# Performance work log

Measured on AMD Instinct MI355X. Metric: run time of the kernel, lower is better.

The kernel has to match this reference:

```python
import jax, jax.numpy as jnp
import numpy as np

B, C, CI, H, W = 4, 256, 128, 64, 64
BN_EPS = 1e-5

def _proj(t, w, b):
    # 1x1 conv == channel-mixing GEMM
    return jnp.einsum('bchw,oc->bohw', t, w) + b[None, :, None, None]

def setup_inputs() -> dict:
    key = jax.random.key(0)
    ks = jax.random.split(key, 16)
    d = {
        'x': jax.random.normal(ks[0], (B, C, H, W), jnp.float32),
        'y': jax.random.normal(ks[1], (B, C, H, W), jnp.float32),
        'z': jax.random.normal(ks[2], (B, C, H, W), jnp.float32),
        'theta_w': jax.random.normal(ks[3], (CI, C), jnp.float32) * 0.02,
        'theta_b': jax.random.normal(ks[4], (CI,), jnp.float32) * 0.02,
        'phi_w': jax.random.normal(ks[5], (CI, C), jnp.float32) * 0.02,
        'phi_b': jax.random.normal(ks[6], (CI,), jnp.float32) * 0.02,
        'g_w': jax.random.normal(ks[7], (CI, C), jnp.float32) * 0.02,
        'g_b': jax.random.normal(ks[8], (CI,), jnp.float32) * 0.02,
        'w_w': jax.random.normal(ks[9], (C, CI), jnp.float32) * 0.02,
        'w_b': jax.random.normal(ks[10], (C,), jnp.float32) * 0.02,
        'bn_gamma': jax.random.normal(ks[11], (C,), jnp.float32) * 0.1 + 1.0,
        'bn_beta': jax.random.normal(ks[12], (C,), jnp.float32) * 0.1,
        'bn_mean': jax.random.normal(ks[13], (C,), jnp.float32) * 0.1,
        'bn_var': jax.random.uniform(ks[14], (C,), jnp.float32, 0.5, 1.5),
    }
    return d

def reference(x, y, z, theta_w, theta_b, phi_w, phi_b, g_w, g_b,
              w_w, w_b, bn_gamma, bn_beta, bn_mean, bn_var):
    b, c, h, w = x.shape
    n = h * w
    theta_x = _proj(x, theta_w, theta_b).reshape(b, CI, n).transpose(0, 2, 1)  # [B,N,Ci]
    phi_y = _proj(y, phi_w, phi_b).reshape(b, CI, n)                           # [B,Ci,N]
    f = jnp.einsum('bnc,bcm->bnm', theta_x, phi_y)                             # [B,N,N]
    f_div_c = jax.nn.softmax(f, axis=-1)
    g_z = _proj(z, g_w, g_b).reshape(b, CI, n).transpose(0, 2, 1)              # [B,N,Ci]
    o = jnp.einsum('bnm,bmc->bnc', f_div_c, g_z)                               # [B,N,Ci]
    o = o.transpose(0, 2, 1).reshape(b, CI, h, w)
    w_y = _proj(o, w_w, w_b)
    # BatchNorm2d (eval mode with running stats)
    inv = bn_gamma / jnp.sqrt(bn_var + BN_EPS)
    w_y = (w_y - bn_mean[None, :, None, None]) * inv[None, :, None, None] + bn_beta[None, :, None, None]
    return w_y + z
```

## Files before the change

### kernel.cpp

```cpp
#include <hip/hip_runtime.h>

typedef unsigned short u16;
typedef unsigned int u32;
typedef short s8v __attribute__((ext_vector_type(8)));
typedef float f16v __attribute__((ext_vector_type(16)));

#define NHW 4096
#define CIN 256
#define CID 128
#define PB  524288

__device__ __forceinline__ u16 f2bf(float f) {
  union { float f; u32 u; } v; v.f = f;
  u32 r = v.u + 0x7fffu + ((v.u >> 16) & 1u);
  return (u16)(r >> 16);
}
__device__ __forceinline__ u32 pk2(float a, float b) {
  return (u32)f2bf(a) | ((u32)f2bf(b) << 16);
}
__device__ __forceinline__ int SIG(int reg, int h) {
  return (reg & 3) + 8 * (reg >> 2) + 4 * h;
}


__global__ __launch_bounds__(256) void wprep_kernel(
    const float* __restrict__ tw, const float* __restrict__ pw, const float* __restrict__ gw,
    const float* __restrict__ ww, const float* __restrict__ wb,
    const float* __restrict__ bg, const float* __restrict__ bb,
    const float* __restrict__ bm, const float* __restrict__ bv,
    u16* __restrict__ Wf, u16* __restrict__ Wf2,
    float* __restrict__ scl, float* __restrict__ offs)
{
  const int bid = blockIdx.x, t = threadIdx.x;
  const int lm = t & 31, h = (t >> 5) & 1, g4 = t >> 6;
  if (bid < 12) {
    const int p = bid >> 2, ct = bid & 3;
    const float* W = (p == 0) ? tw : (p == 1) ? pw : gw;
#pragma unroll
    for (int q = 0; q < 4; ++q) {
      const int ksg = g4 * 4 + q;
      const float* src = W + (size_t)(ct * 32 + lm) * 256 + ksg * 16 + h * 8;
      u32 pk[4];
#pragma unroll
      for (int e = 0; e < 4; ++e) pk[e] = pk2(src[2 * e], src[2 * e + 1]);
      *(uint4*)(Wf + p * 32768 + ct * 8192 + ksg * 512 + h * 256 + lm * 8) =
          make_uint4(pk[0], pk[1], pk[2], pk[3]);
    }
  } else if (bid < 20) {
    const int ct = bid - 12;
#pragma unroll
    for (int q = 0; q < 2; ++q) {
      const int ks = g4 * 2 + q;
      const float* src = ww + (size_t)(ct * 32 + lm) * 128 + ks * 16 + h * 8;
      u32 pk[4];
#pragma unroll
      for (int e = 0; e < 4; ++e) pk[e] = pk2(src[2 * e], src[2 * e + 1]);
      *(uint4*)(Wf2 + ct * 8192 + ks * 512 + h * 256 + lm * 8) =
          make_uint4(pk[0], pk[1], pk[2], pk[3]);
    }
  } else {
    float inv = bg[t] * __frsqrt_rn(bv[t] + 1e-5f);
    scl[t] = inv;
    offs[t] = (wb[t] - bm[t]) * inv + bb[t];
  }
}

__global__ __launch_bounds__(256) void proj_kernel(
    const float* __restrict__ x, const float* __restrict__ y, const float* __restrict__ zz,
    const u16* __restrict__ Wf,
    const float* __restrict__ tb, const float* __restrict__ pb, const float* __restrict__ gb,
    u16* __restrict__ Qf, u16* __restrict__ Kf, u16* __restrict__ Vf)
{
  __shared__ __align__(16) u16 Xs[64 * 64];
  __shared__ float Bs[128];
  const int t = threadIdx.x;
  const int b = blockIdx.y, p = blockIdx.z;
  const int n0 = blockIdx.x * 64;
  const float* in  = (p == 0) ? x  : (p == 1) ? y  : zz;
  const float* Bv  = (p == 0) ? tb : (p == 1) ? pb : gb;
  u16*         out = (p == 0) ? Qf : (p == 1) ? Kf : Vf;
  const u16* Wfp = Wf + p * 32768;

  const int wave = t >> 6, lane = t & 63;
  const int lm = lane & 31, h = lane >> 5;
  const int nt = wave & 1, ctp = wave >> 1;
  const int cp = t >> 3, noct = t & 7;

  if (t < 128) Bs[t] = Bv[t];

  u32* Xd = (u32*)Xs;
  const int nn = nt * 32 + lm;
  const int rmask = ((nn >> 3) & 7) << 2;

  f16v a0, a1;
#pragma unroll
  for (int r = 0; r < 16; ++r) { a0[r] = 0.f; a1[r] = 0.f; }

  float4 xr[4];
  {
    const float* basep = in + ((size_t)(b * CIN) + 2 * cp) * NHW + n0;
    xr[0] = *(const float4*)(basep + noct * 4);
    xr[1] = *(const float4*)(basep + 32 + noct * 4);
    xr[2] = *(const float4*)(basep + NHW + noct * 4);
    xr[3] = *(const float4*)(basep + NHW + 32 + noct * 4);
  }

  for (int ch = 0; ch < 4; ++ch) {
    __syncthreads();
    {
      const float* xa = (const float*)&xr[0];
      const float* xb = (const float*)&xr[1];
      const float* xc = (const float*)&xr[2];
      const float* xd = (const float*)&xr[3];
#pragma unroll
      for (int i = 0; i < 4; ++i) {
        int n1 = noct * 4 + i, n2 = n1 + 32;
        Xd[n1 * 32 + (cp ^ (((n1 >> 3) & 7) << 2))] = pk2(xa[i], xc[i]);
        Xd[n2 * 32 + (cp ^ (((n2 >> 3) & 7) << 2))] = pk2(xb[i], xd[i]);
      }
    }
    __syncthreads();
    if (ch < 3) {
      const float* basep = in + ((size_t)(b * CIN) + (ch + 1) * 64 + 2 * cp) * NHW + n0;
      xr[0] = *(const float4*)(basep + noct * 4);
      xr[1] = *(const float4*)(basep + 32 + noct * 4);
      xr[2] = *(const float4*)(basep + NHW + noct * 4);
      xr[3] = *(const float4*)(basep + NHW + 32 + noct * 4);
    }
    if (p < 2) {
#pragma unroll
      for (int ks = 0; ks < 4; ++ks) {
        s8v xf = *(const s8v*)(Xd + nn * 32 + ((ks * 8 + h * 4) ^ rmask));
        s8v w0 = *(const s8v*)(Wfp + (ctp * 2 + 0) * 8192 + (ch * 4 + ks) * 512 + h * 256 + lm * 8);
        s8v w1 = *(const s8v*)(Wfp + (ctp * 2 + 1) * 8192 + (ch * 4 + ks) * 512 + h * 256 + lm * 8);
        a0 = __builtin_amdgcn_mfma_f32_32x32x16_bf16(w0, xf, a0, 0, 0, 0);
        a1 = __builtin_amdgcn_mfma_f32_32x32x16_bf16(w1, xf, a1, 0, 0, 0);
      }
    } else {
#pragma unroll
      for (int ks = 0; ks < 4; ++ks) {
        s8v xf = *(const s8v*)(Xd + nn * 32 + ((ks * 8 + h * 4) ^ rmask));
        s8v w0 = *(const s8v*)(Wfp + (ctp * 2 + 0) * 8192 + (ch * 4 + ks) * 512 + h * 256 + lm * 8);
        s8v w1 = *(const s8v*)(Wfp + (ctp * 2 + 1) * 8192 + (ch * 4 + ks) * 512 + h * 256 + lm * 8);
        a0 = __builtin_amdgcn_mfma_f32_32x32x16_bf16(xf, w0, a0, 0, 0, 0);
        a1 = __builtin_amdgcn_mfma_f32_32x32x16_bf16(xf, w1, a1, 0, 0, 0);
      }
    }
  }

  const size_t nblk = (size_t)blockIdx.x * 2 + nt;
  if (p < 2) {
#pragma unroll
    for (int cti = 0; cti < 2; ++cti) {
      const int ct = ctp * 2 + cti;
      const f16v& ac = cti ? a1 : a0;
      float v[16];
#pragma unroll
      for (int reg = 0; reg < 16; ++reg) v[reg] = ac[reg] + Bs[ct * 32 + SIG(reg, h)];
      u32 pk[8];
#pragma unroll
      for (int e = 0; e < 8; ++e) pk[e] = pk2(v[2 * e], v[2 * e + 1]);
      u16* dst = out + (size_t)b * PB + nblk * 4096 + ct * 1024 + h * 512 + lm * 16;
      ((uint4*)dst)[0] = make_uint4(pk[0], pk[1], pk[2], pk[3]);
      ((uint4*)dst)[1] = make_uint4(pk[4], pk[5], pk[6], pk[7]);
    }
  } else {
#pragma unroll
    for (int cti = 0; cti < 2; ++cti) {
      const int ct = ctp * 2 + cti;
      const f16v& ac = cti ? a1 : a0;
      const float bias = Bs[ct * 32 + lm];
      u32 pk[8];
#pragma unroll
      for (int e = 0; e < 8; ++e) pk[e] = pk2(ac[2 * e] + bias, ac[2 * e + 1] + bias);
      u16* dst = out + (size_t)b * PB + nblk * 4096 + ct * 1024 + h * 256 + lm * 8;
      *(uint4*)dst         = make_uint4(pk[0], pk[1], pk[2], pk[3]);
      *(uint4*)(dst + 512) = make_uint4(pk[4], pk[5], pk[6], pk[7]);
    }
  }
}

__global__ __launch_bounds__(256, 2) void attn_kernel(
    const u16* __restrict__ Qf, const u16* __restrict__ Kf,
    const u16* __restrict__ Vf, u16* __restrict__ Of)
{
  __shared__ __align__(16) float Obuf[32][132];
  __shared__ float lbuf[32];
  const int t = threadIdx.x;
  const int wave = t >> 6, lane = t & 63;
  const int lm = lane & 31, half = lane >> 5;
  const int b = blockIdx.y;

  s8v qf[8];
  {
    const u16* qp = Qf + (size_t)b * PB + (size_t)blockIdx.x * 4096 + lm * 16 + half * 8;
#pragma unroll
    for (int ks = 0; ks < 8; ++ks) qf[ks] = *(const s8v*)(qp + ks * 512);
  }

  const u16* Kb = Kf + (size_t)b * PB + lm * 16 + half * 8;
  const u16* Vb = Vf + (size_t)b * PB + half * 256 + lm * 8;
  const int mstart = wave * 1024;

  f16v oacc[4];
#pragma unroll
  for (int c = 0; c < 4; ++c)
#pragma unroll
    for (int r = 0; r < 16; ++r) oacc[c][r] = 0.f;
  float lacc = 0.f;

  s8v kf[8];
  {
    const u16* kp = Kb + (size_t)mstart * 128;
#pragma unroll
    for (int ks = 0; ks < 8; ++ks) kf[ks] = *(const s8v*)(kp + ks * 512);
  }

  for (int jt = 0; jt < 32; ++jt) {
    const int m0 = mstart + jt * 32;

    s8v vf[8];
    {
      const u16* vp = Vb + (size_t)m0 * 128;
#pragma unroll
      for (int ct = 0; ct < 4; ++ct)
#pragma unroll
        for (int ks = 0; ks < 2; ++ks)
          vf[ct * 2 + ks] = *(const s8v*)(vp + ct * 1024 + ks * 512);
    }

    f16v sacc;
#pragma unroll
    for (int r = 0; r < 16; ++r) sacc[r] = 0.f;
#pragma unroll
    for (int ks = 0; ks < 8; ++ks)
      sacc = __builtin_amdgcn_mfma_f32_32x32x16_bf16(kf[ks], qf[ks], sacc, 0, 0, 0);

    {
      const u16* kp = Kb + (size_t)(m0 + 32) * 128;
#pragma unroll
      for (int ks = 0; ks < 8; ++ks) kf[ks] = *(const s8v*)(kp + ks * 512);
    }

    union { s8v v; u16 e[8]; } pa0, pa1;
#pragma unroll
    for (int j = 0; j < 8; ++j) {
      float p0 = __expf(sacc[j]);
      float p1 = __expf(sacc[8 + j]);
      lacc += p0 + p1;
      pa0.e[j] = f2bf(p0);
      pa1.e[j] = f2bf(p1);
    }

#pragma unroll
    for (int ct = 0; ct < 4; ++ct) {
      oacc[ct] = __builtin_amdgcn_mfma_f32_32x32x16_bf16(pa0.v, vf[ct * 2 + 0], oacc[ct], 0, 0, 0);
      oacc[ct] = __builtin_amdgcn_mfma_f32_32x32x16_bf16(pa1.v, vf[ct * 2 + 1], oacc[ct], 0, 0, 0);
    }
  }

  lacc += __shfl_xor(lacc, 32);

  __syncthreads();
  if (wave == 0) {
#pragma unroll
    for (int ct = 0; ct < 4; ++ct)
#pragma unroll
      for (int reg = 0; reg < 16; ++reg)
        Obuf[SIG(reg, half)][ct * 32 + lm] = oacc[ct][reg];
    if (half == 0) lbuf[lm] = lacc;
  }
  __syncthreads();
  if (wave != 0) {
#pragma unroll
    for (int ct = 0; ct < 4; ++ct)
#pragma unroll
      for (int reg = 0; reg < 16; ++reg)
        atomicAdd(&Obuf[SIG(reg, half)][ct * 32 + lm], oacc[ct][reg]);
    if (half == 0) atomicAdd(&lbuf[lm], lacc);
  }
  __syncthreads();

  {
    const float inv = 1.0f / lbuf[lm];
    u16* ob = Of + (size_t)b * PB + (size_t)blockIdx.x * 4096 + half * 256 + lm * 8;
#pragma unroll
    for (int kss = 0; kss < 2; ++kss) {
      const int ks = wave * 2 + kss;
      float4 va = *(const float4*)&Obuf[lm][ks * 16 + half * 8];
      float4 vb = *(const float4*)&Obuf[lm][ks * 16 + half * 8 + 4];
      uint4 pk = make_uint4(pk2(va.x * inv, va.y * inv), pk2(va.z * inv, va.w * inv),
                            pk2(vb.x * inv, vb.y * inv), pk2(vb.z * inv, vb.w * inv));
      *(uint4*)(ob + ks * 512) = pk;
    }
  }
}

__global__ __launch_bounds__(256) void outproj_kernel(
    const u16* __restrict__ Of, const float* __restrict__ zz,
    const u16* __restrict__ Wf2, const float* __restrict__ scl,
    const float* __restrict__ offs, float* __restrict__ out)
{
  __shared__ float SC[256], OFS[256];
  const int t = threadIdx.x;
  const int wave = t >> 6, lane = t & 63;
  const int lm = lane & 31, h = lane >> 5;
  const int b = blockIdx.y;
  const int n0 = blockIdx.x * 32;

  SC[t] = scl[t];
  OFS[t] = offs[t];
  __syncthreads();

  s8v of[8];
  {
    const u16* op = Of + (size_t)b * PB + (size_t)blockIdx.x * 4096 + h * 256 + lm * 8;
#pragma unroll
    for (int ks = 0; ks < 8; ++ks) of[ks] = *(const s8v*)(op + ks * 512);
  }

  f16v a0, a1;
#pragma unroll
  for (int r = 0; r < 16; ++r) { a0[r] = 0.f; a1[r] = 0.f; }

  const u16* w2a = Wf2 + (wave * 2 + 0) * 8192 + h * 256 + lm * 8;
  const u16* w2b = Wf2 + (wave * 2 + 1) * 8192 + h * 256 + lm * 8;
#pragma unroll
  for (int ks = 0; ks < 8; ++ks) {
    s8v wa = *(const s8v*)(w2a + ks * 512);
    s8v wb = *(const s8v*)(w2b + ks * 512);
    a0 = __builtin_amdgcn_mfma_f32_32x32x16_bf16(wa, of[ks], a0, 0, 0, 0);
    a1 = __builtin_amdgcn_mfma_f32_32x32x16_bf16(wb, of[ks], a1, 0, 0, 0);
  }

#pragma unroll
  for (int cti = 0; cti < 2; ++cti) {
    const int ct = wave * 2 + cti;
    const f16v& ac = cti ? a1 : a0;
#pragma unroll
    for (int reg = 0; reg < 16; ++reg) {
      const int co = ct * 32 + SIG(reg, h);
      const size_t idx = ((size_t)(b * CIN + co)) * NHW + n0 + lm;
      out[idx] = ac[reg] * SC[co] + OFS[co] + zz[idx];
    }
  }
}

extern "C" void kernel_launch(void* const* d_in, const int* in_sizes, int n_in,
                              void* d_out, int out_size, void* d_ws, size_t ws_size,
                              hipStream_t stream) {
  const float* x  = (const float*)d_in[0];
  const float* y  = (const float*)d_in[1];
  const float* z  = (const float*)d_in[2];
  const float* tw = (const float*)d_in[3];
  const float* tb = (const float*)d_in[4];
  const float* pw = (const float*)d_in[5];
  const float* pb = (const float*)d_in[6];
  const float* gw = (const float*)d_in[7];
  const float* gb = (const float*)d_in[8];
  const float* ww = (const float*)d_in[9];
  const float* wb = (const float*)d_in[10];
  const float* bn_g = (const float*)d_in[11];
  const float* bn_b = (const float*)d_in[12];
  const float* bn_m = (const float*)d_in[13];
  const float* bn_v = (const float*)d_in[14];

  const size_t B = 4;
  const size_t qkv = B * PB;
  char* ws = (char*)d_ws;
  u16* Qf = (u16*)ws;
  u16* Kf = Qf + qkv;
  u16* Vf = Kf + qkv;
  u16* Of = Vf + qkv;
  u16* Wf = Of + qkv;
  u16* Wf2 = Wf + 3 * 32768;
  float* scl  = (float*)(Wf2 + 65536);
  float* offs = scl + 256;

  float* out = (float*)d_out;

  wprep_kernel<<<21, 256, 0, stream>>>(tw, pw, gw, ww, wb, bn_g, bn_b, bn_m, bn_v,
                                       Wf, Wf2, scl, offs);
  proj_kernel<<<dim3(NHW / 64, B, 3), 256, 0, stream>>>(
      x, y, z, Wf, tb, pb, gb, Qf, Kf, Vf);
  attn_kernel<<<dim3(NHW / 32, B), 256, 0, stream>>>(Qf, Kf, Vf, Of);
  outproj_kernel<<<dim3(NHW / 32, B), 256, 0, stream>>>(
      Of, z, Wf2, scl, offs, out);
}
```

Measured before the change: 202.0 us.

## Pre-convert inputs to bf16 fragments and split attention over 8 waves

Adds an xprep kernel that converts x, y, z to bf16 in MFMA fragment layout through an LDS transpose. The projection kernel then loads operands straight from global memory, with no LDS staging or barriers. Separately, the attention kernel moves from 256 to 512 threads, so each wave covers half as many key tiles and the epilogue stores are spread across 8 waves. The cost is an extra kernel launch, an extra round trip of the converted inputs through memory, and more atomic reductions in LDS; the output buffer and the X workspace are reused as scratch.

```diff
diff --git a/kernel.cpp b/kernel.cpp
--- a/kernel.cpp
+++ b/kernel.cpp
@@ -9,6 +9,7 @@
 #define CIN 256
 #define CID 128
 #define PB  524288
+#define XSZ 1048576
 
 __device__ __forceinline__ u16 f2bf(float f) {
   union { float f; u32 u; } v; v.f = f;
@@ -65,86 +66,84 @@
   }
 }
 
+__global__ __launch_bounds__(256) void xprep_kernel(
+    const float* __restrict__ x, const float* __restrict__ y, const float* __restrict__ zz,
+    u16* __restrict__ X0, u16* __restrict__ X1, u16* __restrict__ X2)
+{
+  __shared__ __align__(16) float Xs[128][68];
+  const int t = threadIdx.x;
+  const int b = blockIdx.y, p = blockIdx.z;
+  const int n0 = blockIdx.x * 64;
+  const float* in = (p == 0) ? x : (p == 1) ? y : zz;
+  u16* Xf = ((p == 0) ? X0 : (p == 1) ? X1 : X2) + (size_t)b * XSZ +
+            (size_t)blockIdx.x * 2 * 8192;
+  const int lm = t & 31, h = (t >> 5) & 1, nb = (t >> 6) & 1, q = t >> 7;
+  const int cr = t >> 4, ns = t & 15;
+
+  for (int pass = 0; pass < 2; ++pass) {
+    if (pass) __syncthreads();
+#pragma unroll
+    for (int is = 0; is < 8; ++is) {
+      int c = pass * 128 + is * 16 + cr;
+      *(float4*)&Xs[is * 16 + cr][ns * 4] =
+          *(const float4*)(in + (size_t)(b * CIN + c) * NHW + n0 + ns * 4);
+    }
+    __syncthreads();
+#pragma unroll
+    for (int i = 0; i < 4; ++i) {
+      const int ksgl = q * 4 + i;
+      const int c0 = ksgl * 16 + h * 8;
+      float v[8];
+#pragma unroll
+      for (int j = 0; j < 8; ++j) v[j] = Xs[c0 + j][nb * 32 + lm];
+      uint4 pk = make_uint4(pk2(v[0], v[1]), pk2(v[2], v[3]),
+                            pk2(v[4], v[5]), pk2(v[6], v[7]));
+      *(uint4*)(Xf + nb * 8192 + (pass * 8 + ksgl) * 512 + h * 256 + lm * 8) = pk;
+    }
+  }
+}
+
 __global__ __launch_bounds__(256) void proj_kernel(
-    const float* __restrict__ x, const float* __restrict__ y, const float* __restrict__ zz,
+    const u16* __restrict__ X0, const u16* __restrict__ X1, const u16* __restrict__ X2,
     const u16* __restrict__ Wf,
     const float* __restrict__ tb, const float* __restrict__ pb, const float* __restrict__ gb,
     u16* __restrict__ Qf, u16* __restrict__ Kf, u16* __restrict__ Vf)
 {
-  __shared__ __align__(16) u16 Xs[64 * 64];
   __shared__ float Bs[128];
   const int t = threadIdx.x;
   const int b = blockIdx.y, p = blockIdx.z;
-  const int n0 = blockIdx.x * 64;
-  const float* in  = (p == 0) ? x  : (p == 1) ? y  : zz;
-  const float* Bv  = (p == 0) ? tb : (p == 1) ? pb : gb;
-  u16*         out = (p == 0) ? Qf : (p == 1) ? Kf : Vf;
-  const u16* Wfp = Wf + p * 32768;
-
-  const int wave = t >> 6, lane = t & 63;
-  const int lm = lane & 31, h = lane >> 5;
-  const int nt = wave & 1, ctp = wave >> 1;
-  const int cp = t >> 3, noct = t & 7;
-
+  const float* Bv = (p == 0) ? tb : (p == 1) ? pb : gb;
+  u16* out = (p == 0) ? Qf : (p == 1) ? Kf : Vf;
+  const int wave = t >> 6, lane = t & 63, lm = lane & 31, h = lane >> 5;
+  const int nt = wave & 1, cih = wave >> 1;
   if (t < 128) Bs[t] = Bv[t];
-
-  u32* Xd = (u32*)Xs;
-  const int nn = nt * 32 + lm;
-  const int rmask = ((nn >> 3) & 7) << 2;
+  __syncthreads();
+
+  const u16* Xb = ((p == 0) ? X0 : (p == 1) ? X1 : X2) + (size_t)b * XSZ +
+                  ((size_t)blockIdx.x * 2 + nt) * 8192 + lane * 8;
+  const u16* Wb = Wf + p * 32768 + cih * 2 * 8192 + lane * 8;
 
   f16v a0, a1;
 #pragma unroll
   for (int r = 0; r < 16; ++r) { a0[r] = 0.f; a1[r] = 0.f; }
 
-  float4 xr[4];
-  {
-    const float* basep = in + ((size_t)(b * CIN) + 2 * cp) * NHW + n0;
-    xr[0] = *(const float4*)(basep + noct * 4);
-    xr[1] = *(const float4*)(basep + 32 + noct * 4);
-    xr[2] = *(const float4*)(basep + NHW + noct * 4);
-    xr[3] = *(const float4*)(basep + NHW + 32 + noct * 4);
-  }
-
-  for (int ch = 0; ch < 4; ++ch) {
-    __syncthreads();
-    {
-      const float* xa = (const float*)&xr[0];
-      const float* xb = (const float*)&xr[1];
-      const float* xc = (const float*)&xr[2];
-      const float* xd = (const float*)&xr[3];
-#pragma unroll
-      for (int i = 0; i < 4; ++i) {
-        int n1 = noct * 4 + i, n2 = n1 + 32;
-        Xd[n1 * 32 + (cp ^ (((n1 >> 3) & 7) << 2))] = pk2(xa[i], xc[i]);
-        Xd[n2 * 32 + (cp ^ (((n2 >> 3) & 7) << 2))] = pk2(xb[i], xd[i]);
-      }
-    }
-    __syncthreads();
-    if (ch < 3) {
-      const float* basep = in + ((size_t)(b * CIN) + (ch + 1) * 64 + 2 * cp) * NHW + n0;
-      xr[0] = *(const float4*)(basep + noct * 4);
-      xr[1] = *(const float4*)(basep + 32 + noct * 4);
-      xr[2] = *(const float4*)(basep + NHW + noct * 4);
-      xr[3] = *(const float4*)(basep + NHW + 32 + noct * 4);
-    }
-    if (p < 2) {
-#pragma unroll
-      for (int ks = 0; ks < 4; ++ks) {
-        s8v xf = *(const s8v*)(Xd + nn * 32 + ((ks * 8 + h * 4) ^ rmask));
-        s8v w0 = *(const s8v*)(Wfp + (ctp * 2 + 0) * 8192 + (ch * 4 + ks) * 512 + h * 256 + lm * 8);
-        s8v w1 = *(const s8v*)(Wfp + (ctp * 2 + 1) * 8192 + (ch * 4 + ks) * 512 + h * 256 + lm * 8);
-        a0 = __builtin_amdgcn_mfma_f32_32x32x16_bf16(w0, xf, a0, 0, 0, 0);
-        a1 = __builtin_amdgcn_mfma_f32_32x32x16_bf16(w1, xf, a1, 0, 0, 0);
-      }
-    } else {
-#pragma unroll
-      for (int ks = 0; ks < 4; ++ks) {
-        s8v xf = *(const s8v*)(Xd + nn * 32 + ((ks * 8 + h * 4) ^ rmask));
-        s8v w0 = *(const s8v*)(Wfp + (ctp * 2 + 0) * 8192 + (ch * 4 + ks) * 512 + h * 256 + lm * 8);
-        s8v w1 = *(const s8v*)(Wfp + (ctp * 2 + 1) * 8192 + (ch * 4 + ks) * 512 + h * 256 + lm * 8);
-        a0 = __builtin_amdgcn_mfma_f32_32x32x16_bf16(xf, w0, a0, 0, 0, 0);
-        a1 = __builtin_amdgcn_mfma_f32_32x32x16_bf16(xf, w1, a1, 0, 0, 0);
-      }
+  if (p < 2) {
+#pragma unroll 4
+    for (int ksg = 0; ksg < 16; ++ksg) {
+      s8v xf = *(const s8v*)(Xb + ksg * 512);
+      s8v w0 = *(const s8v*)(Wb + ksg * 512);
+      s8v w1 = *(const s8v*)(Wb + 8192 + ksg * 512);
+      a0 = __builtin_amdgcn_mfma_f32_32x32x16_bf16(w0, xf, a0, 0, 0, 0);
+      a1 = __builtin_amdgcn_mfma_f32_32x32x16_bf16(w1, xf, a1, 0, 0, 0);
+    }
+  } else {
+#pragma unroll 4
+    for (int ksg = 0; ksg < 16; ++ksg) {
+      s8v xf = *(const s8v*)(Xb + ksg * 512);
+      s8v w0 = *(const s8v*)(Wb + ksg * 512);
+      s8v w1 = *(const s8v*)(Wb + 8192 + ksg * 512);
+      a0 = __builtin_amdgcn_mfma_f32_32x32x16_bf16(xf, w0, a0, 0, 0, 0);
+      a1 = __builtin_amdgcn_mfma_f32_32x32x16_bf16(xf, w1, a1, 0, 0, 0);
     }
   }
 
@@ -152,7 +151,7 @@
   if (p < 2) {
 #pragma unroll
     for (int cti = 0; cti < 2; ++cti) {
-      const int ct = ctp * 2 + cti;
+      const int ct = cih * 2 + cti;
       const f16v& ac = cti ? a1 : a0;
       float v[16];
 #pragma unroll
@@ -167,7 +166,7 @@
   } else {
 #pragma unroll
     for (int cti = 0; cti < 2; ++cti) {
-      const int ct = ctp * 2 + cti;
+      const int ct = cih * 2 + cti;
       const f16v& ac = cti ? a1 : a0;
       const float bias = Bs[ct * 32 + lm];
       u32 pk[8];
@@ -180,7 +179,7 @@
   }
 }
 
-__global__ __launch_bounds__(256, 2) void attn_kernel(
+__global__ __launch_bounds__(512, 4) void attn_kernel(
     const u16* __restrict__ Qf, const u16* __restrict__ Kf,
     const u16* __restrict__ Vf, u16* __restrict__ Of)
 {
@@ -200,7 +199,7 @@
 
   const u16* Kb = Kf + (size_t)b * PB + lm * 16 + half * 8;
   const u16* Vb = Vf + (size_t)b * PB + half * 256 + lm * 8;
-  const int mstart = wave * 1024;
+  const int mstart = wave * 512;
 
   f16v oacc[4];
 #pragma unroll
@@ -216,7 +215,7 @@
     for (int ks = 0; ks < 8; ++ks) kf[ks] = *(const s8v*)(kp + ks * 512);
   }
 
-  for (int jt = 0; jt < 32; ++jt) {
+  for (int jt = 0; jt < 16; ++jt) {
     const int m0 = mstart + jt * 32;
 
     s8v vf[8];
@@ -284,15 +283,11 @@
   {
     const float inv = 1.0f / lbuf[lm];
     u16* ob = Of + (size_t)b * PB + (size_t)blockIdx.x * 4096 + half * 256 + lm * 8;
-#pragma unroll
-    for (int kss = 0; kss < 2; ++kss) {
-      const int ks = wave * 2 + kss;
-      float4 va = *(const float4*)&Obuf[lm][ks * 16 + half * 8];
-      float4 vb = *(const float4*)&Obuf[lm][ks * 16 + half * 8 + 4];
-      uint4 pk = make_uint4(pk2(va.x * inv, va.y * inv), pk2(va.z * inv, va.w * inv),
-                            pk2(vb.x * inv, vb.y * inv), pk2(vb.z * inv, vb.w * inv));
-      *(uint4*)(ob + ks * 512) = pk;
-    }
+    float4 va = *(const float4*)&Obuf[lm][wave * 16 + half * 8];
+    float4 vb = *(const float4*)&Obuf[lm][wave * 16 + half * 8 + 4];
+    uint4 pk = make_uint4(pk2(va.x * inv, va.y * inv), pk2(va.z * inv, va.w * inv),
+                          pk2(vb.x * inv, vb.y * inv), pk2(vb.z * inv, vb.w * inv));
+    *(uint4*)(ob + wave * 512) = pk;
   }
 }
 
@@ -366,24 +361,27 @@
   const float* bn_v = (const float*)d_in[14];
 
   const size_t B = 4;
-  const size_t qkv = B * PB;
   char* ws = (char*)d_ws;
-  u16* Qf = (u16*)ws;
-  u16* Kf = Qf + qkv;
-  u16* Vf = Kf + qkv;
-  u16* Of = Vf + qkv;
-  u16* Wf = Of + qkv;
+  u16* Qf  = (u16*)ws;
+  u16* Kf  = Qf + 4 * (size_t)PB;
+  u16* Vf  = Kf + 4 * (size_t)PB;
+  u16* XfA = Vf + 4 * (size_t)PB;
+  u16* XfB = XfA + 4 * (size_t)XSZ;
+  u16* Wf  = XfB + 4 * (size_t)XSZ;
   u16* Wf2 = Wf + 3 * 32768;
   float* scl  = (float*)(Wf2 + 65536);
   float* offs = scl + 256;
+  u16* XfC = (u16*)d_out;
+  u16* Of  = XfA;
 
   float* out = (float*)d_out;
 
   wprep_kernel<<<21, 256, 0, stream>>>(tw, pw, gw, ww, wb, bn_g, bn_b, bn_m, bn_v,
                                        Wf, Wf2, scl, offs);
+  xprep_kernel<<<dim3(NHW / 64, B, 3), 256, 0, stream>>>(x, y, z, XfA, XfB, XfC);
   proj_kernel<<<dim3(NHW / 64, B, 3), 256, 0, stream>>>(
-      x, y, z, Wf, tb, pb, gb, Qf, Kf, Vf);
-  attn_kernel<<<dim3(NHW / 32, B), 256, 0, stream>>>(Qf, Kf, Vf, Of);
+      XfA, XfB, XfC, Wf, tb, pb, gb, Qf, Kf, Vf);
+  attn_kernel<<<dim3(NHW / 32, B), 512, 0, stream>>>(Qf, Kf, Vf, Of);
   outproj_kernel<<<dim3(NHW / 32, B), 256, 0, stream>>>(
       Of, z, Wf2, scl, offs, out);
 }
```

Result: slower. 281.8 us (+39.5%).
